# Performance work log

Measured on AMD Instinct MI355X. Metric: run time of the kernel, lower is better.

## Reference

```python
import jax, jax.numpy as jnp
import numpy as np

N, E, M, C = 4000, 60000, 16, 64        # nodes, edges, (lmax+1)^2, sphere_channels
H, HEADS, A, VC, CE, Z = 64, 8, 8, 8, 32, 90  # attn hidden, heads, alpha ch, value ch, edge ch, max elements


def _params(key):
    ks = jax.random.split(key, 10)
    g = lambda k, sh, fan: jax.random.normal(k, sh, dtype=jnp.float32) / np.float32(np.sqrt(fan))
    return [g(ks[0], (Z, CE), CE),          # emb_s: source atom embedding
            g(ks[1], (Z, CE), CE),          # emb_t: target atom embedding
            g(ks[2], (CE,), 1.0),           # w_d : distance projection
            g(ks[3], (CE, H), CE),          # We  : edge scalar -> hidden (m=0 inject)
            g(ks[4], (C, H), C),            # Ws  : source channel mix
            g(ks[5], (C, H), C),            # Wt  : target channel mix
            g(ks[6], (H, HEADS * A), H),    # Wa  : alpha features
            g(ks[7], (HEADS, A), A),        # va  : per-head alpha vector
            g(ks[8], (H, HEADS * VC), H),   # Wv  : values
            g(ks[9], (HEADS * VC, 1), HEADS * VC)]  # Wo : output proj (1 channel)


def setup_inputs() -> dict:
    key = jax.random.key(0)
    ks = jax.random.split(key, 8)
    x = jax.random.normal(ks[0], (N, M, C), dtype=jnp.float32)
    atomic_numbers = jax.random.randint(ks[1], (N,), 0, Z)
    edge_distance = jax.random.uniform(ks[2], (E,), dtype=jnp.float32) * 5.0 + 0.5
    edge_index = jax.random.randint(ks[3], (2, E), 0, N)
    noise_mask = jax.random.randint(ks[4], (N,), 0, 2).astype(bool)
    # per-edge SO3/Wigner rotation: random orthogonal [E, M, M]
    rng = np.random.default_rng(0)
    q, _ = np.linalg.qr(rng.standard_normal((E, M, M)).astype(np.float32))
    wigner = jnp.asarray(q, dtype=jnp.float32)
    names = ['emb_s', 'emb_t', 'w_d', 'We', 'Ws', 'Wt', 'Wa', 'va', 'Wv', 'Wo']
    inp = {'x': x, 'atomic_numbers': atomic_numbers, 'edge_distance': edge_distance,
           'edge_index': edge_index, 'noise_mask': noise_mask, 'wigner': wigner}
    for n, v in zip(names, _params(ks[5])):
        inp['fs_' + n] = v
    for n, v in zip(names, _params(ks[6])):
        inp['dn_' + n] = v
    return inp


def _block(x, zn, dist, src, dst, D, emb_s, emb_t, w_d, We, Ws, Wt, Wa, va, Wv, Wo):
    # gather + rotate edge-wise node features into edge-aligned frame
    xs = jnp.einsum('emn,enc->emc', D, x[src])            # [E,M,C]
    xt = jnp.einsum('emn,enc->emc', D, x[dst])            # [E,M,C]
    # scalar edge embedding (distance + source/target atom embeddings)
    e = jax.nn.silu(dist[:, None] * w_d + emb_s[zn[src]] + emb_t[zn[dst]])  # [E,CE]
    # SO2-style channel mixing; inject edge scalars into the m=0 (invariant) row
    f = jnp.einsum('emc,ch->emh', xs, Ws) + jnp.einsum('emc,ch->emh', xt, Wt)  # [E,M,H]
    f = f.at[:, 0, :].add(e @ We)
    # attention logits from the invariant part
    a = jax.nn.leaky_relu(f[:, 0, :] @ Wa, 0.2).reshape(E, HEADS, A)
    logits = jnp.einsum('eha,ha->eh', a, va)              # [E,HEADS]
    # segment softmax over incoming edges per target node
    mx = jax.ops.segment_max(logits, dst, num_segments=N)
    ex = jnp.exp(logits - mx[dst])
    alpha = ex / (jax.ops.segment_sum(ex, dst, num_segments=N)[dst] + 1e-9)
    # values, attention-weight, rotate back (D^T), scatter to nodes
    v = (f @ Wv).reshape(E, M, HEADS, VC) * alpha[:, None, :, None]
    v = jnp.einsum('emn,emhv->enhv', D, v).reshape(E, M, HEADS * VC)
    out = jax.ops.segment_sum(v, dst, num_segments=N) @ Wo  # [N,M,1]
    return out[:, 1:4, 0]  # narrow(1, 1, 3) -> l=1 vector components [N,3]


def reference(x, atomic_numbers, edge_distance, edge_index, noise_mask, wigner,
              fs_emb_s, fs_emb_t, fs_w_d, fs_We, fs_Ws, fs_Wt, fs_Wa, fs_va, fs_Wv, fs_Wo,
              dn_emb_s, dn_emb_t, dn_w_d, dn_We, dn_Ws, dn_Wt, dn_Wa, dn_va, dn_Wv, dn_Wo):
    src, dst = edge_index[0], edge_index[1]
    forces = _block(x, atomic_numbers, edge_distance, src, dst, wigner,
                    fs_emb_s, fs_emb_t, fs_w_d, fs_We, fs_Ws, fs_Wt, fs_Wa, fs_va, fs_Wv, fs_Wo)
    den = _block(x, atomic_numbers, edge_distance, src, dst, wigner,
                 dn_emb_s, dn_emb_t, dn_w_d, dn_We, dn_Ws, dn_Wt, dn_Wa, dn_va, dn_Wv, dn_Wo)
    # denoising_pos_forward with noise_mask: forces = den*mask + forces*~mask
    m = noise_mask[:, None].astype(x.dtype)
    return den * m + forces * (1.0 - m)
```

## Files before the change

### kernel.cpp

```cpp
#include <hip/hip_runtime.h>

typedef unsigned short ushort_t;
typedef __attribute__((ext_vector_type(8))) short short8;
typedef __attribute__((ext_vector_type(4))) float floatx4;

constexpr int RS = 11520;

__device__ inline float bf2f(ushort_t u) {
    union { unsigned int i; float f; } v; v.i = ((unsigned int)u) << 16; return v.f;
}
__device__ inline ushort_t f2bf(float f) {
    union { float f; unsigned int i; } v; v.f = f;
    unsigned int b = v.i + 0x7FFFu + ((v.i >> 16) & 1u);
    return (ushort_t)(b >> 16);
}

__global__ __launch_bounds__(256) void k_composites(
    const float* __restrict__ Ws0, const float* __restrict__ Wt0, const float* __restrict__ We0,
    const float* __restrict__ Wa0, const float* __restrict__ Wv0, const float* __restrict__ Wo0,
    const float* __restrict__ Ws1, const float* __restrict__ Wt1, const float* __restrict__ We1,
    const float* __restrict__ Wa1, const float* __restrict__ Wv1, const float* __restrict__ Wo1,
    float* __restrict__ cmp, ushort_t* __restrict__ packW)
{
    int task = blockIdx.x;
    int r    = blockIdx.y;
    int z    = blockIdx.z;
    const float* Ws = r ? Ws1 : Ws0;
    const float* Wt = r ? Wt1 : Wt0;
    const float* We = r ? We1 : We0;
    const float* Wa = r ? Wa1 : Wa0;
    const float* Wv = r ? Wv1 : Wv0;
    const float* Wo = r ? Wo1 : Wo0;
    float* base = cmp + r * RS;

    if (task == 0 || task == 1) {
        const float* L = task ? Wt : Ws;
        ushort_t* pw = packW + (r * 2 + task) * 4096;
        int lo = z * 1024;
        for (int idx = lo + threadIdx.x; idx < lo + 1024; idx += 256) {
            int c = idx >> 6, jc = idx & 63;
            float a = 0.f;
            #pragma unroll 8
            for (int k = 0; k < 64; ++k) a += L[c * 64 + k] * Wa[k * 64 + jc];
            int t = jc >> 4, n = jc & 15, kh = c >> 5, q = (c >> 3) & 3, jj = c & 7;
            pw[((t * 2 + kh) * 64 + q * 16 + n) * 8 + jj] = f2bf(a);
        }
    } else if (task == 2) {
        float* out = base + 8192;
        int lo = z * 512;
        for (int idx = lo + threadIdx.x; idx < lo + 512; idx += 256) {
            int ce = idx >> 6, jc = idx & 63;
            float a = 0.f;
            #pragma unroll 8
            for (int k = 0; k < 64; ++k) a += We[ce * 64 + k] * Wa[k * 64 + jc];
            out[idx] = a;
        }
    } else {
        if (z != 0) return;
        const float* L = (task == 3) ? Ws : (task == 4) ? Wt : We;
        int rows = (task == 5) ? 32 : 64;
        float* out = base + ((task == 3) ? 10240 : (task == 4) ? 10752 : 11264);
        for (int idx = threadIdx.x; idx < rows * 8; idx += 256) {
            int c = idx >> 3, h = idx & 7;
            float a = 0.f;
            for (int k = 0; k < 64; ++k) {
                float wv = 0.f;
                #pragma unroll
                for (int aa = 0; aa < 8; ++aa) wv += Wv[k * 64 + h * 8 + aa] * Wo[h * 8 + aa];
                a += L[c * 64 + k] * wv;
            }
            out[idx] = a;
        }
    }
}

__device__ inline short8 bfragP(const float* __restrict__ P0, const float* __restrict__ P1,
                                int kBase, int q, int n) {
    const float* P = (n < 8) ? P0 : P1;
    int c = n & 7;
    short8 f;
    #pragma unroll
    for (int j = 0; j < 8; ++j)
        f[j] = (short)f2bf(P[(kBase + q * 8 + j) * 8 + c]);
    return f;
}
__device__ inline void st4(ushort_t* dst, const floatx4& c) {
    uint2 v;
    v.x = (unsigned int)f2bf(c[0]) | ((unsigned int)f2bf(c[1]) << 16);
    v.y = (unsigned int)f2bf(c[2]) | ((unsigned int)f2bf(c[3]) << 16);
    *(uint2*)dst = v;
}

#define MFMA(a, b, c) __builtin_amdgcn_mfma_f32_16x16x32_bf16((a), (b), (c), 0, 0, 0)

__global__ __launch_bounds__(256, 2) void k_node(
    const float* __restrict__ x, const int* __restrict__ mask,
    const float* __restrict__ cmp, const ushort_t* __restrict__ packW,
    float* __restrict__ psrc, float* __restrict__ ptgt,
    ushort_t* __restrict__ srcA, ushort_t* __restrict__ tgtA,
    float* __restrict__ den, float* __restrict__ num,
    int N, int totWaves)
{
    int wid  = (int)((blockIdx.x * blockDim.x + threadIdx.x) >> 6);
    int lane = threadIdx.x & 63;
    int q    = lane >> 4;
    int n16  = lane & 15;

    short8 Bs0[4][2], Bs1[4][2], Bt0[4][2], Bt1[4][2];
    #pragma unroll
    for (int t = 0; t < 4; ++t) {
        #pragma unroll
        for (int kh = 0; kh < 2; ++kh) {
            int fo = (t * 2 + kh) * 512 + lane * 8;
            Bs0[t][kh] = *(const short8*)(packW +           fo);
            Bt0[t][kh] = *(const short8*)(packW +  4096 +   fo);
            Bs1[t][kh] = *(const short8*)(packW +  8192 +   fo);
            Bt1[t][kh] = *(const short8*)(packW + 12288 +   fo);
        }
    }
    short8 Bp[2], Bq[2];
    #pragma unroll
    for (int kh = 0; kh < 2; ++kh) {
        Bp[kh] = bfragP(cmp + 10240, cmp + RS + 10240, kh * 32, q, n16);
        Bq[kh] = bfragP(cmp + 10752, cmp + RS + 10752, kh * 32, q, n16);
    }

    const floatx4 zero = {0.f, 0.f, 0.f, 0.f};

    for (int nd = wid; nd < N; nd += totWaves) {
        if (lane < 8)  den[nd * 8 + lane] = 0.f;
        if (lane < 24) num[nd * 24 + lane] = 0.f;

        const float* xp = x + (size_t)nd * 1024 + n16 * 64 + q * 8;
        float4 v0 = *(const float4*)(xp);
        float4 v1 = *(const float4*)(xp + 4);
        float4 v2 = *(const float4*)(xp + 32);
        float4 v3 = *(const float4*)(xp + 36);
        short8 a0, a1;
        a0[0] = (short)f2bf(v0.x); a0[1] = (short)f2bf(v0.y);
        a0[2] = (short)f2bf(v0.z); a0[3] = (short)f2bf(v0.w);
        a0[4] = (short)f2bf(v1.x); a0[5] = (short)f2bf(v1.y);
        a0[6] = (short)f2bf(v1.z); a0[7] = (short)f2bf(v1.w);
        a1[0] = (short)f2bf(v2.x); a1[1] = (short)f2bf(v2.y);
        a1[2] = (short)f2bf(v2.z); a1[3] = (short)f2bf(v2.w);
        a1[4] = (short)f2bf(v3.x); a1[5] = (short)f2bf(v3.y);
        a1[6] = (short)f2bf(v3.z); a1[7] = (short)f2bf(v3.w);

        int rsel = (mask[nd] != 0);

        {
            floatx4 c0 = zero, c1 = zero, c2 = zero, c3 = zero;
            c0 = MFMA(a0, Bs0[0][0], c0); c0 = MFMA(a1, Bs0[0][1], c0);
            c1 = MFMA(a0, Bs0[1][0], c1); c1 = MFMA(a1, Bs0[1][1], c1);
            c2 = MFMA(a0, Bs0[2][0], c2); c2 = MFMA(a1, Bs0[2][1], c2);
            c3 = MFMA(a0, Bs0[3][0], c3); c3 = MFMA(a1, Bs0[3][1], c3);
            ushort_t* sp = srcA + (size_t)nd * 2048 + n16 * 16 + q * 4;
            st4(sp, c0); st4(sp + 256, c1); st4(sp + 512, c2); st4(sp + 768, c3);
        }
        {
            floatx4 c0 = zero, c1 = zero, c2 = zero, c3 = zero;
            c0 = MFMA(a0, Bs1[0][0], c0); c0 = MFMA(a1, Bs1[0][1], c0);
            c1 = MFMA(a0, Bs1[1][0], c1); c1 = MFMA(a1, Bs1[1][1], c1);
            c2 = MFMA(a0, Bs1[2][0], c2); c2 = MFMA(a1, Bs1[2][1], c2);
            c3 = MFMA(a0, Bs1[3][0], c3); c3 = MFMA(a1, Bs1[3][1], c3);
            ushort_t* sp = srcA + (size_t)nd * 2048 + 1024 + n16 * 16 + q * 4;
            st4(sp, c0); st4(sp + 256, c1); st4(sp + 512, c2); st4(sp + 768, c3);
        }

        {
            floatx4 c0 = zero, c1 = zero, c2 = zero, c3 = zero;
            if (rsel) {
                c0 = MFMA(a0, Bt1[0][0], c0); c0 = MFMA(a1, Bt1[0][1], c0);
                c1 = MFMA(a0, Bt1[1][0], c1); c1 = MFMA(a1, Bt1[1][1], c1);
                c2 = MFMA(a0, Bt1[2][0], c2); c2 = MFMA(a1, Bt1[2][1], c2);
                c3 = MFMA(a0, Bt1[3][0], c3); c3 = MFMA(a1, Bt1[3][1], c3);
            } else {
                c0 = MFMA(a0, Bt0[0][0], c0); c0 = MFMA(a1, Bt0[0][1], c0);
                c1 = MFMA(a0, Bt0[1][0], c1); c1 = MFMA(a1, Bt0[1][1], c1);
                c2 = MFMA(a0, Bt0[2][0], c2); c2 = MFMA(a1, Bt0[2][1], c2);
                c3 = MFMA(a0, Bt0[3][0], c3); c3 = MFMA(a1, Bt0[3][1], c3);
            }
            ushort_t* tp = tgtA + (size_t)nd * 1024 + n16 * 16 + q * 4;
            st4(tp, c0); st4(tp + 256, c1); st4(tp + 512, c2); st4(tp + 768, c3);
        }

        {
            floatx4 cp = zero;
            cp = MFMA(a0, Bp[0], cp); cp = MFMA(a1, Bp[1], cp);
            if (q == 0) {
                int r = n16 >> 3, h = n16 & 7;
                float* pp = psrc + (size_t)nd * 48 + r * 24 + h;
                pp[0]  = cp[1];
                pp[8]  = cp[2];
                pp[16] = cp[3];
            }
            floatx4 cq = zero;
            cq = MFMA(a0, Bq[0], cq); cq = MFMA(a1, Bq[1], cq);
            if (q == 0 && (n16 >> 3) == rsel) {
                int h = n16 & 7;
                float* pp = ptgt + (size_t)nd * 24 + h;
                pp[0]  = cq[1];
                pp[8]  = cq[2];
                pp[16] = cq[3];
            }
        }
    }
}

__global__ __launch_bounds__(256) void k_fused(
    const int* __restrict__ ei, const float* __restrict__ dist,
    const int* __restrict__ zn, const int* __restrict__ mask,
    const float* __restrict__ wig, const float* __restrict__ cmp,
    const float* __restrict__ embs0, const float* __restrict__ embt0, const float* __restrict__ wd0,
    const float* __restrict__ embs1, const float* __restrict__ embt1, const float* __restrict__ wd1,
    const float* __restrict__ va0, const float* __restrict__ va1,
    const ushort_t* __restrict__ srcA, const ushort_t* __restrict__ tgtA,
    const float* __restrict__ psrc, const float* __restrict__ ptgt,
    float* __restrict__ den, float* __restrict__ num, int E)
{
    int wv = threadIdx.x >> 6, j = threadIdx.x & 63;
    int e = blockIdx.x * 4 + wv;
    if (e >= E) return;
    int src = ei[e], dst = ei[E + e];
    int r = (mask[dst] != 0);
    float d = dist[e];
    int zs = zn[src], zt = zn[dst];
    int hq = j >> 3, h8 = j & 7;

    const float* w0 = wig + (size_t)e * 256;
    float4 wA = *(const float4*)(w0);
    float4 wB = *(const float4*)(w0 + 4);
    float4 wC = *(const float4*)(w0 + 8);
    float4 wD = *(const float4*)(w0 + 12);
    const ushort_t* sa = srcA + (size_t)src * 2048 + r * 1024 + j * 16;
    const ushort_t* ta = tgtA + (size_t)dst * 1024 + j * 16;
    short8 sv0 = *(const short8*)(sa);
    short8 sv1 = *(const short8*)(sa + 8);
    short8 tv0 = *(const short8*)(ta);
    short8 tv1 = *(const short8*)(ta + 8);
    float pv = 0.f;
    if (h8 < 3)
        pv = psrc[(size_t)src * 48 + r * 24 + h8 * 8 + hq]
           + ptgt[(size_t)dst * 24 + h8 * 8 + hq];

    float es;
    {
        int ce = j & 31;
        float z = r ? (d * wd1[ce] + embs1[zs * 32 + ce] + embt1[zt * 32 + ce])
                    : (d * wd0[ce] + embs0[zs * 32 + ce] + embt0[zt * 32 + ce]);
        es = z / (1.f + __expf(-z));
    }

    const float* WeWa   = cmp + r * RS + 8192;
    const float* WeWvWo = cmp + r * RS + 11264;
    float f0a = 0.f, ej = 0.f;
    #pragma unroll
    for (int ce = 0; ce < 32; ++ce) {
        float ev = __shfl(es, ce, 64);
        f0a += ev * WeWa[ce * 64 + j];
        ej  += ev * WeWvWo[ce * 8 + hq];
    }

    f0a += wA.x * (bf2f((ushort_t)sv0[0]) + bf2f((ushort_t)tv0[0]));
    f0a += wA.y * (bf2f((ushort_t)sv0[1]) + bf2f((ushort_t)tv0[1]));
    f0a += wA.z * (bf2f((ushort_t)sv0[2]) + bf2f((ushort_t)tv0[2]));
    f0a += wA.w * (bf2f((ushort_t)sv0[3]) + bf2f((ushort_t)tv0[3]));
    f0a += wB.x * (bf2f((ushort_t)sv0[4]) + bf2f((ushort_t)tv0[4]));
    f0a += wB.y * (bf2f((ushort_t)sv0[5]) + bf2f((ushort_t)tv0[5]));
    f0a += wB.z * (bf2f((ushort_t)sv0[6]) + bf2f((ushort_t)tv0[6]));
    f0a += wB.w * (bf2f((ushort_t)sv0[7]) + bf2f((ushort_t)tv0[7]));
    f0a += wC.x * (bf2f((ushort_t)sv1[0]) + bf2f((ushort_t)tv1[0]));
    f0a += wC.y * (bf2f((ushort_t)sv1[1]) + bf2f((ushort_t)tv1[1]));
    f0a += wC.z * (bf2f((ushort_t)sv1[2]) + bf2f((ushort_t)tv1[2]));
    f0a += wC.w * (bf2f((ushort_t)sv1[3]) + bf2f((ushort_t)tv1[3]));
    f0a += wD.x * (bf2f((ushort_t)sv1[4]) + bf2f((ushort_t)tv1[4]));
    f0a += wD.y * (bf2f((ushort_t)sv1[5]) + bf2f((ushort_t)tv1[5]));
    f0a += wD.z * (bf2f((ushort_t)sv1[6]) + bf2f((ushort_t)tv1[6]));
    f0a += wD.w * (bf2f((ushort_t)sv1[7]) + bf2f((ushort_t)tv1[7]));

    float la = f0a > 0.f ? f0a : 0.2f * f0a;
    float val = la * (r ? va1[j] : va0[j]);
    val += __shfl_xor(val, 1);
    val += __shfl_xor(val, 2);
    val += __shfl_xor(val, 4);
    float ex = __expf(val);

    if (h8 == 0) atomicAdd(&den[dst * 8 + hq], ex);
    if (h8 < 3) {
        float w0k = (h8 == 0) ? wA.y : (h8 == 1) ? wA.z : wA.w;
        atomicAdd(&num[dst * 24 + hq * 3 + h8], ex * (pv + ej * w0k));
    }
}

__global__ __launch_bounds__(256) void k_out(
    const float* __restrict__ num, const float* __restrict__ den,
    float* __restrict__ out, int N3)
{
    int t = blockIdx.x * 256 + threadIdx.x;
    if (t >= N3) return;
    int n = t / 3, k = t - n * 3;
    float acc = 0.f;
    #pragma unroll
    for (int h = 0; h < 8; ++h)
        acc += num[n * 24 + h * 3 + k] / (den[n * 8 + h] + 1e-9f);
    out[t] = acc;
}

extern "C" void kernel_launch(void* const* d_in, const int* in_sizes, int n_in,
                              void* d_out, int out_size, void* d_ws, size_t ws_size,
                              hipStream_t stream) {
    const float* x    = (const float*)d_in[0];
    const int*   zn   = (const int*)d_in[1];
    const float* dist = (const float*)d_in[2];
    const int*   ei   = (const int*)d_in[3];
    const int*   mask = (const int*)d_in[4];
    const float* wig  = (const float*)d_in[5];
    const float* fs[10]; const float* dn[10];
    for (int i = 0; i < 10; ++i) { fs[i] = (const float*)d_in[6 + i]; dn[i] = (const float*)d_in[16 + i]; }

    int N = in_sizes[1];
    int E = in_sizes[2];

    float* cmp  = (float*)d_ws;
    float* den  = cmp + 2 * RS;
    float* num  = den + (size_t)N * 8;
    float* psrc = num + (size_t)N * 24;
    float* ptgt = psrc + (size_t)N * 48;
    ushort_t* srcA = (ushort_t*)(ptgt + (size_t)N * 24);
    ushort_t* tgtA = srcA + (size_t)N * 2048;
    ushort_t* packW = tgtA + (size_t)N * 1024;


    k_composites<<<dim3(6, 2, 4), 256, 0, stream>>>(
        fs[4], fs[5], fs[3], fs[6], fs[8], fs[9],
        dn[4], dn[5], dn[3], dn[6], dn[8], dn[9], cmp, packW);

    int nodeBlocks = 1000;
    int totWaves = nodeBlocks * (256 / 64);
    k_node<<<nodeBlocks, 256, 0, stream>>>(x, mask, cmp, packW, psrc, ptgt,
                                           srcA, tgtA, den, num, N, totWaves);

    k_fused<<<(E + 3) / 4, 256, 0, stream>>>(
        ei, dist, zn, mask, wig, cmp,
        fs[0], fs[1], fs[2], dn[0], dn[1], dn[2],
        fs[7], dn[7], srcA, tgtA, psrc, ptgt, den, num, E);

    k_out<<<(N * 3 + 255) / 256, 256, 0, stream>>>(num, den, (float*)d_out, N * 3);
}
```

Baseline: 225.1 us.

## Sort edges by destination in cooperative prep kernel and stage node weights in LDS

Replaces the weight-composite kernel with a cooperative kernel that also computes a counting sort of edges by destination node, so the edge kernel visits edges in dst order. This improves locality of the atomic accumulation into den/num and of the target-node gathers. The node kernel now stages packed bf16 weights in shared memory instead of holding them in registers, and uses one wave per node with higher occupancy. The cost is three grid syncs, global atomics for binning, and an extra indirection per edge.

```diff
diff --git a/kernel.cpp b/kernel.cpp
--- a/kernel.cpp
+++ b/kernel.cpp
@@ -1,4 +1,7 @@
 #include <hip/hip_runtime.h>
+#include <hip/hip_cooperative_groups.h>
+
+namespace cg = cooperative_groups;
 
 typedef unsigned short ushort_t;
 typedef __attribute__((ext_vector_type(8))) short short8;
@@ -13,76 +16,6 @@
     union { float f; unsigned int i; } v; v.f = f;
     unsigned int b = v.i + 0x7FFFu + ((v.i >> 16) & 1u);
     return (ushort_t)(b >> 16);
-}
-
-__global__ __launch_bounds__(256) void k_composites(
-    const float* __restrict__ Ws0, const float* __restrict__ Wt0, const float* __restrict__ We0,
-    const float* __restrict__ Wa0, const float* __restrict__ Wv0, const float* __restrict__ Wo0,
-    const float* __restrict__ Ws1, const float* __restrict__ Wt1, const float* __restrict__ We1,
-    const float* __restrict__ Wa1, const float* __restrict__ Wv1, const float* __restrict__ Wo1,
-    float* __restrict__ cmp, ushort_t* __restrict__ packW)
-{
-    int task = blockIdx.x;
-    int r    = blockIdx.y;
-    int z    = blockIdx.z;
-    const float* Ws = r ? Ws1 : Ws0;
-    const float* Wt = r ? Wt1 : Wt0;
-    const float* We = r ? We1 : We0;
-    const float* Wa = r ? Wa1 : Wa0;
-    const float* Wv = r ? Wv1 : Wv0;
-    const float* Wo = r ? Wo1 : Wo0;
-    float* base = cmp + r * RS;
-
-    if (task == 0 || task == 1) {
-        const float* L = task ? Wt : Ws;
-        ushort_t* pw = packW + (r * 2 + task) * 4096;
-        int lo = z * 1024;
-        for (int idx = lo + threadIdx.x; idx < lo + 1024; idx += 256) {
-            int c = idx >> 6, jc = idx & 63;
-            float a = 0.f;
-            #pragma unroll 8
-            for (int k = 0; k < 64; ++k) a += L[c * 64 + k] * Wa[k * 64 + jc];
-            int t = jc >> 4, n = jc & 15, kh = c >> 5, q = (c >> 3) & 3, jj = c & 7;
-            pw[((t * 2 + kh) * 64 + q * 16 + n) * 8 + jj] = f2bf(a);
-        }
-    } else if (task == 2) {
-        float* out = base + 8192;
-        int lo = z * 512;
-        for (int idx = lo + threadIdx.x; idx < lo + 512; idx += 256) {
-            int ce = idx >> 6, jc = idx & 63;
-            float a = 0.f;
-            #pragma unroll 8
-            for (int k = 0; k < 64; ++k) a += We[ce * 64 + k] * Wa[k * 64 + jc];
-            out[idx] = a;
-        }
-    } else {
-        if (z != 0) return;
-        const float* L = (task == 3) ? Ws : (task == 4) ? Wt : We;
-        int rows = (task == 5) ? 32 : 64;
-        float* out = base + ((task == 3) ? 10240 : (task == 4) ? 10752 : 11264);
-        for (int idx = threadIdx.x; idx < rows * 8; idx += 256) {
-            int c = idx >> 3, h = idx & 7;
-            float a = 0.f;
-            for (int k = 0; k < 64; ++k) {
-                float wv = 0.f;
-                #pragma unroll
-                for (int aa = 0; aa < 8; ++aa) wv += Wv[k * 64 + h * 8 + aa] * Wo[h * 8 + aa];
-                a += L[c * 64 + k] * wv;
-            }
-            out[idx] = a;
-        }
-    }
-}
-
-__device__ inline short8 bfragP(const float* __restrict__ P0, const float* __restrict__ P1,
-                                int kBase, int q, int n) {
-    const float* P = (n < 8) ? P0 : P1;
-    int c = n & 7;
-    short8 f;
-    #pragma unroll
-    for (int j = 0; j < 8; ++j)
-        f[j] = (short)f2bf(P[(kBase + q * 8 + j) * 8 + c]);
-    return f;
 }
 __device__ inline void st4(ushort_t* dst, const floatx4& c) {
     uint2 v;
@@ -93,41 +26,133 @@
 
 #define MFMA(a, b, c) __builtin_amdgcn_mfma_f32_16x16x32_bf16((a), (b), (c), 0, 0, 0)
 
-__global__ __launch_bounds__(256, 2) void k_node(
+__global__ __launch_bounds__(256) void k_pre(
+    const float* __restrict__ Ws0, const float* __restrict__ Wt0, const float* __restrict__ We0,
+    const float* __restrict__ Wa0, const float* __restrict__ Wv0, const float* __restrict__ Wo0,
+    const float* __restrict__ Ws1, const float* __restrict__ Wt1, const float* __restrict__ We1,
+    const float* __restrict__ Wa1, const float* __restrict__ Wv1, const float* __restrict__ Wo1,
+    const int* __restrict__ ei, float* __restrict__ cmp, ushort_t* __restrict__ packW,
+    int* __restrict__ binCnt, int* __restrict__ binPos, int* __restrict__ order,
+    int N, int E)
+{
+    cg::grid_group g = cg::this_grid();
+    __shared__ int part[256];
+    int tid = blockIdx.x * 256 + threadIdx.x;
+    int nT  = gridDim.x * 256;
+
+    for (int i = tid; i < N; i += nT) binCnt[i] = 0;
+    g.sync();
+    for (int e = tid; e < E; e += nT) atomicAdd(&binCnt[ei[E + e]], 1);
+    g.sync();
+
+    int b = blockIdx.x;
+    if (b < 48) {
+        int task = b % 6, r = (b / 6) % 2, z = b / 12;
+        const float* Ws = r ? Ws1 : Ws0;
+        const float* Wt = r ? Wt1 : Wt0;
+        const float* We = r ? We1 : We0;
+        const float* Wa = r ? Wa1 : Wa0;
+        const float* Wv = r ? Wv1 : Wv0;
+        const float* Wo = r ? Wo1 : Wo0;
+        float* base = cmp + r * RS;
+
+        if (task == 0 || task == 1) {
+            const float* L = task ? Wt : Ws;
+            ushort_t* pw = packW + (r * 2 + task) * 4096;
+            int lo = z * 1024;
+            for (int idx = lo + threadIdx.x; idx < lo + 1024; idx += 256) {
+                int c = idx >> 6, jc = idx & 63;
+                float a = 0.f;
+                #pragma unroll 8
+                for (int k = 0; k < 64; ++k) a += L[c * 64 + k] * Wa[k * 64 + jc];
+                int t = jc >> 4, n = jc & 15, kh = c >> 5, q = (c >> 3) & 3, jj = c & 7;
+                pw[((t * 2 + kh) * 64 + q * 16 + n) * 8 + jj] = f2bf(a);
+            }
+        } else if (task == 2) {
+            float* out = base + 8192;
+            int lo = z * 512;
+            for (int idx = lo + threadIdx.x; idx < lo + 512; idx += 256) {
+                int ce = idx >> 6, jc = idx & 63;
+                float a = 0.f;
+                #pragma unroll 8
+                for (int k = 0; k < 64; ++k) a += We[ce * 64 + k] * Wa[k * 64 + jc];
+                out[idx] = a;
+            }
+        } else if (z == 0) {
+            if (task == 5) {
+                float* out = base + 11264;
+                for (int idx = threadIdx.x; idx < 32 * 8; idx += 256) {
+                    int c = idx >> 3, h = idx & 7;
+                    float a = 0.f;
+                    for (int k = 0; k < 64; ++k) {
+                        float wv = 0.f;
+                        #pragma unroll
+                        for (int aa = 0; aa < 8; ++aa) wv += Wv[k * 64 + h * 8 + aa] * Wo[h * 8 + aa];
+                        a += We[c * 64 + k] * wv;
+                    }
+                    out[idx] = a;
+                }
+            } else {
+                const float* L = (task == 3) ? Ws : Wt;
+                ushort_t* pp = packW + 16384 + (task - 3) * 1024;
+                for (int idx = threadIdx.x; idx < 64 * 8; idx += 256) {
+                    int c = idx >> 3, h = idx & 7;
+                    float a = 0.f;
+                    for (int k = 0; k < 64; ++k) {
+                        float wv = 0.f;
+                        #pragma unroll
+                        for (int aa = 0; aa < 8; ++aa) wv += Wv[k * 64 + h * 8 + aa] * Wo[h * 8 + aa];
+                        a += L[c * 64 + k] * wv;
+                    }
+                    int kh = c >> 5, q = (c >> 3) & 3, jj = c & 7;
+                    pp[kh * 512 + (q * 16 + r * 8 + h) * 8 + jj] = f2bf(a);
+                }
+            }
+        }
+    } else if (b == 48) {
+        int t = threadIdx.x;
+        int chunk = (N + 255) / 256;
+        int lo = t * chunk, hi = lo + chunk; if (hi > N) hi = N; if (lo > N) lo = N;
+        int s = 0;
+        for (int i = lo; i < hi; ++i) s += binCnt[i];
+        part[t] = s;
+        __syncthreads();
+        for (int off = 1; off < 256; off <<= 1) {
+            int v = (t >= off) ? part[t - off] : 0;
+            __syncthreads();
+            part[t] += v;
+            __syncthreads();
+        }
+        int start = (t == 0) ? 0 : part[t - 1];
+        for (int i = lo; i < hi; ++i) { int c = binCnt[i]; binPos[i] = start; start += c; }
+    }
+    g.sync();
+
+    for (int e = tid; e < E; e += nT) {
+        int pos = atomicAdd(&binPos[ei[E + e]], 1);
+        order[pos] = e;
+    }
+}
+
+__global__ __launch_bounds__(256, 4) void k_node(
     const float* __restrict__ x, const int* __restrict__ mask,
-    const float* __restrict__ cmp, const ushort_t* __restrict__ packW,
+    const ushort_t* __restrict__ packW,
     float* __restrict__ psrc, float* __restrict__ ptgt,
     ushort_t* __restrict__ srcA, ushort_t* __restrict__ tgtA,
-    float* __restrict__ den, float* __restrict__ num,
-    int N, int totWaves)
+    float* __restrict__ den, float* __restrict__ num, int N)
 {
+    __shared__ __align__(16) ushort_t lw[18432];
+    for (int i = threadIdx.x; i < 2304; i += 256)
+        ((short8*)lw)[i] = ((const short8*)packW)[i];
+    __syncthreads();
+
     int wid  = (int)((blockIdx.x * blockDim.x + threadIdx.x) >> 6);
     int lane = threadIdx.x & 63;
     int q    = lane >> 4;
     int n16  = lane & 15;
 
-    short8 Bs0[4][2], Bs1[4][2], Bt0[4][2], Bt1[4][2];
-    #pragma unroll
-    for (int t = 0; t < 4; ++t) {
-        #pragma unroll
-        for (int kh = 0; kh < 2; ++kh) {
-            int fo = (t * 2 + kh) * 512 + lane * 8;
-            Bs0[t][kh] = *(const short8*)(packW +           fo);
-            Bt0[t][kh] = *(const short8*)(packW +  4096 +   fo);
-            Bs1[t][kh] = *(const short8*)(packW +  8192 +   fo);
-            Bt1[t][kh] = *(const short8*)(packW + 12288 +   fo);
-        }
-    }
-    short8 Bp[2], Bq[2];
-    #pragma unroll
-    for (int kh = 0; kh < 2; ++kh) {
-        Bp[kh] = bfragP(cmp + 10240, cmp + RS + 10240, kh * 32, q, n16);
-        Bq[kh] = bfragP(cmp + 10752, cmp + RS + 10752, kh * 32, q, n16);
-    }
-
-    const floatx4 zero = {0.f, 0.f, 0.f, 0.f};
-
-    for (int nd = wid; nd < N; nd += totWaves) {
+    if (wid < N) {
+        int nd = wid;
         if (lane < 8)  den[nd * 8 + lane] = 0.f;
         if (lane < 24) num[nd * 24 + lane] = 0.f;
 
@@ -147,46 +172,42 @@
         a1[6] = (short)f2bf(v3.z); a1[7] = (short)f2bf(v3.w);
 
         int rsel = (mask[nd] != 0);
+        const floatx4 zero = {0.f, 0.f, 0.f, 0.f};
+
+        #define WF(mat, t, kh) (*(const short8*)&lw[(mat) * 4096 + ((t) * 2 + (kh)) * 512 + lane * 8])
+        #define PF(m, kh)      (*(const short8*)&lw[16384 + (m) * 1024 + (kh) * 512 + lane * 8])
 
         {
             floatx4 c0 = zero, c1 = zero, c2 = zero, c3 = zero;
-            c0 = MFMA(a0, Bs0[0][0], c0); c0 = MFMA(a1, Bs0[0][1], c0);
-            c1 = MFMA(a0, Bs0[1][0], c1); c1 = MFMA(a1, Bs0[1][1], c1);
-            c2 = MFMA(a0, Bs0[2][0], c2); c2 = MFMA(a1, Bs0[2][1], c2);
-            c3 = MFMA(a0, Bs0[3][0], c3); c3 = MFMA(a1, Bs0[3][1], c3);
+            c0 = MFMA(a0, WF(0,0,0), c0); c0 = MFMA(a1, WF(0,0,1), c0);
+            c1 = MFMA(a0, WF(0,1,0), c1); c1 = MFMA(a1, WF(0,1,1), c1);
+            c2 = MFMA(a0, WF(0,2,0), c2); c2 = MFMA(a1, WF(0,2,1), c2);
+            c3 = MFMA(a0, WF(0,3,0), c3); c3 = MFMA(a1, WF(0,3,1), c3);
             ushort_t* sp = srcA + (size_t)nd * 2048 + n16 * 16 + q * 4;
             st4(sp, c0); st4(sp + 256, c1); st4(sp + 512, c2); st4(sp + 768, c3);
         }
         {
             floatx4 c0 = zero, c1 = zero, c2 = zero, c3 = zero;
-            c0 = MFMA(a0, Bs1[0][0], c0); c0 = MFMA(a1, Bs1[0][1], c0);
-            c1 = MFMA(a0, Bs1[1][0], c1); c1 = MFMA(a1, Bs1[1][1], c1);
-            c2 = MFMA(a0, Bs1[2][0], c2); c2 = MFMA(a1, Bs1[2][1], c2);
-            c3 = MFMA(a0, Bs1[3][0], c3); c3 = MFMA(a1, Bs1[3][1], c3);
+            c0 = MFMA(a0, WF(2,0,0), c0); c0 = MFMA(a1, WF(2,0,1), c0);
+            c1 = MFMA(a0, WF(2,1,0), c1); c1 = MFMA(a1, WF(2,1,1), c1);
+            c2 = MFMA(a0, WF(2,2,0), c2); c2 = MFMA(a1, WF(2,2,1), c2);
+            c3 = MFMA(a0, WF(2,3,0), c3); c3 = MFMA(a1, WF(2,3,1), c3);
             ushort_t* sp = srcA + (size_t)nd * 2048 + 1024 + n16 * 16 + q * 4;
             st4(sp, c0); st4(sp + 256, c1); st4(sp + 512, c2); st4(sp + 768, c3);
         }
-
         {
+            int mt = rsel ? 3 : 1;
             floatx4 c0 = zero, c1 = zero, c2 = zero, c3 = zero;
-            if (rsel) {
-                c0 = MFMA(a0, Bt1[0][0], c0); c0 = MFMA(a1, Bt1[0][1], c0);
-                c1 = MFMA(a0, Bt1[1][0], c1); c1 = MFMA(a1, Bt1[1][1], c1);
-                c2 = MFMA(a0, Bt1[2][0], c2); c2 = MFMA(a1, Bt1[2][1], c2);
-                c3 = MFMA(a0, Bt1[3][0], c3); c3 = MFMA(a1, Bt1[3][1], c3);
-            } else {
-                c0 = MFMA(a0, Bt0[0][0], c0); c0 = MFMA(a1, Bt0[0][1], c0);
-                c1 = MFMA(a0, Bt0[1][0], c1); c1 = MFMA(a1, Bt0[1][1], c1);
-                c2 = MFMA(a0, Bt0[2][0], c2); c2 = MFMA(a1, Bt0[2][1], c2);
-                c3 = MFMA(a0, Bt0[3][0], c3); c3 = MFMA(a1, Bt0[3][1], c3);
-            }
+            c0 = MFMA(a0, WF(mt,0,0), c0); c0 = MFMA(a1, WF(mt,0,1), c0);
+            c1 = MFMA(a0, WF(mt,1,0), c1); c1 = MFMA(a1, WF(mt,1,1), c1);
+            c2 = MFMA(a0, WF(mt,2,0), c2); c2 = MFMA(a1, WF(mt,2,1), c2);
+            c3 = MFMA(a0, WF(mt,3,0), c3); c3 = MFMA(a1, WF(mt,3,1), c3);
             ushort_t* tp = tgtA + (size_t)nd * 1024 + n16 * 16 + q * 4;
             st4(tp, c0); st4(tp + 256, c1); st4(tp + 512, c2); st4(tp + 768, c3);
         }
-
         {
             floatx4 cp = zero;
-            cp = MFMA(a0, Bp[0], cp); cp = MFMA(a1, Bp[1], cp);
+            cp = MFMA(a0, PF(0,0), cp); cp = MFMA(a1, PF(0,1), cp);
             if (q == 0) {
                 int r = n16 >> 3, h = n16 & 7;
                 float* pp = psrc + (size_t)nd * 48 + r * 24 + h;
@@ -195,7 +216,7 @@
                 pp[16] = cp[3];
             }
             floatx4 cq = zero;
-            cq = MFMA(a0, Bq[0], cq); cq = MFMA(a1, Bq[1], cq);
+            cq = MFMA(a0, PF(1,0), cq); cq = MFMA(a1, PF(1,1), cq);
             if (q == 0 && (n16 >> 3) == rsel) {
                 int h = n16 & 7;
                 float* pp = ptgt + (size_t)nd * 24 + h;
@@ -204,10 +225,12 @@
                 pp[16] = cq[3];
             }
         }
-    }
-}
-
-__global__ __launch_bounds__(256) void k_fused(
+        #undef WF
+        #undef PF
+    }
+}
+
+__global__ __launch_bounds__(256, 8) void k_fused(
     const int* __restrict__ ei, const float* __restrict__ dist,
     const int* __restrict__ zn, const int* __restrict__ mask,
     const float* __restrict__ wig, const float* __restrict__ cmp,
@@ -216,11 +239,13 @@
     const float* __restrict__ va0, const float* __restrict__ va1,
     const ushort_t* __restrict__ srcA, const ushort_t* __restrict__ tgtA,
     const float* __restrict__ psrc, const float* __restrict__ ptgt,
+    const int* __restrict__ order,
     float* __restrict__ den, float* __restrict__ num, int E)
 {
     int wv = threadIdx.x >> 6, j = threadIdx.x & 63;
-    int e = blockIdx.x * 4 + wv;
-    if (e >= E) return;
+    int el = blockIdx.x * 4 + wv;
+    if (el >= E) return;
+    int e = order[el];
     int src = ei[e], dst = ei[E + e];
     int r = (mask[dst] != 0);
     float d = dist[e];
@@ -329,21 +354,26 @@
     ushort_t* srcA = (ushort_t*)(ptgt + (size_t)N * 24);
     ushort_t* tgtA = srcA + (size_t)N * 2048;
     ushort_t* packW = tgtA + (size_t)N * 1024;
-
-
-    k_composites<<<dim3(6, 2, 4), 256, 0, stream>>>(
-        fs[4], fs[5], fs[3], fs[6], fs[8], fs[9],
-        dn[4], dn[5], dn[3], dn[6], dn[8], dn[9], cmp, packW);
-
-    int nodeBlocks = 1000;
-    int totWaves = nodeBlocks * (256 / 64);
-    k_node<<<nodeBlocks, 256, 0, stream>>>(x, mask, cmp, packW, psrc, ptgt,
-                                           srcA, tgtA, den, num, N, totWaves);
+    int* binCnt = (int*)(packW + 18432);
+    int* binPos = binCnt + N;
+    int* order  = binPos + N;
+
+    const float *Ws0 = fs[4], *Wt0 = fs[5], *We0 = fs[3], *Wa0 = fs[6], *Wv0 = fs[8], *Wo0 = fs[9];
+    const float *Ws1 = dn[4], *Wt1 = dn[5], *We1 = dn[3], *Wa1 = dn[6], *Wv1 = dn[8], *Wo1 = dn[9];
+    int Nv = N, Ev = E;
+    void* args[] = { &Ws0, &Wt0, &We0, &Wa0, &Wv0, &Wo0,
+                     &Ws1, &Wt1, &We1, &Wa1, &Wv1, &Wo1,
+                     &ei, &cmp, &packW, &binCnt, &binPos, &order, &Nv, &Ev };
+    hipLaunchCooperativeKernel((const void*)k_pre, dim3(256), dim3(256), args, 0, stream);
+
+    int nodeBlocks = (N + 3) / 4;
+    k_node<<<nodeBlocks, 256, 0, stream>>>(x, mask, packW, psrc, ptgt,
+                                           srcA, tgtA, den, num, N);
 
     k_fused<<<(E + 3) / 4, 256, 0, stream>>>(
         ei, dist, zn, mask, wig, cmp,
         fs[0], fs[1], fs[2], dn[0], dn[1], dn[2],
-        fs[7], dn[7], srcA, tgtA, psrc, ptgt, den, num, E);
+        fs[7], dn[7], srcA, tgtA, psrc, ptgt, order, den, num, E);
 
     k_out<<<(N * 3 + 255) / 256, 256, 0, stream>>>(num, den, (float*)d_out, N * 3);
 }
```

Result: slower. 447.5 us (+98.8%).

## Make edge kernel persistent with software-prefetched next-edge loads

Applied to the files above, without the earlier changes.

The per-edge kernel becomes a grid-stride persistent loop over a fixed 2048-block grid. Each wave prefetches the next edge's Wigner row, gathered node features, projections and embeddings while it computes the current edge, and loads indices two edges ahead. The aim is to hide gather latency and cut block launch overhead. In exchange, register pressure rises and fewer waves are resident, which may reduce the latency hiding that occupancy used to provide.

```diff
diff --git a/kernel.cpp b/kernel.cpp
--- a/kernel.cpp
+++ b/kernel.cpp
@@ -14,6 +14,14 @@
     unsigned int b = v.i + 0x7FFFu + ((v.i >> 16) & 1u);
     return (ushort_t)(b >> 16);
 }
+__device__ inline void st4(ushort_t* dst, const floatx4& c) {
+    uint2 v;
+    v.x = (unsigned int)f2bf(c[0]) | ((unsigned int)f2bf(c[1]) << 16);
+    v.y = (unsigned int)f2bf(c[2]) | ((unsigned int)f2bf(c[3]) << 16);
+    *(uint2*)dst = v;
+}
+
+#define MFMA(a, b, c) __builtin_amdgcn_mfma_f32_16x16x32_bf16((a), (b), (c), 0, 0, 0)
 
 __global__ __launch_bounds__(256) void k_composites(
     const float* __restrict__ Ws0, const float* __restrict__ Wt0, const float* __restrict__ We0,
@@ -84,14 +92,6 @@
         f[j] = (short)f2bf(P[(kBase + q * 8 + j) * 8 + c]);
     return f;
 }
-__device__ inline void st4(ushort_t* dst, const floatx4& c) {
-    uint2 v;
-    v.x = (unsigned int)f2bf(c[0]) | ((unsigned int)f2bf(c[1]) << 16);
-    v.y = (unsigned int)f2bf(c[2]) | ((unsigned int)f2bf(c[3]) << 16);
-    *(uint2*)dst = v;
-}
-
-#define MFMA(a, b, c) __builtin_amdgcn_mfma_f32_16x16x32_bf16((a), (b), (c), 0, 0, 0)
 
 __global__ __launch_bounds__(256, 2) void k_node(
     const float* __restrict__ x, const int* __restrict__ mask,
@@ -166,7 +166,6 @@
             ushort_t* sp = srcA + (size_t)nd * 2048 + 1024 + n16 * 16 + q * 4;
             st4(sp, c0); st4(sp + 256, c1); st4(sp + 512, c2); st4(sp + 768, c3);
         }
-
         {
             floatx4 c0 = zero, c1 = zero, c2 = zero, c3 = zero;
             if (rsel) {
@@ -183,7 +182,6 @@
             ushort_t* tp = tgtA + (size_t)nd * 1024 + n16 * 16 + q * 4;
             st4(tp, c0); st4(tp + 256, c1); st4(tp + 512, c2); st4(tp + 768, c3);
         }
-
         {
             floatx4 cp = zero;
             cp = MFMA(a0, Bp[0], cp); cp = MFMA(a1, Bp[1], cp);
@@ -216,79 +214,123 @@
     const float* __restrict__ va0, const float* __restrict__ va1,
     const ushort_t* __restrict__ srcA, const ushort_t* __restrict__ tgtA,
     const float* __restrict__ psrc, const float* __restrict__ ptgt,
-    float* __restrict__ den, float* __restrict__ num, int E)
+    float* __restrict__ den, float* __restrict__ num, int E, int stride)
 {
     int wv = threadIdx.x >> 6, j = threadIdx.x & 63;
-    int e = blockIdx.x * 4 + wv;
-    if (e >= E) return;
-    int src = ei[e], dst = ei[E + e];
-    int r = (mask[dst] != 0);
-    float d = dist[e];
-    int zs = zn[src], zt = zn[dst];
-    int hq = j >> 3, h8 = j & 7;
-
-    const float* w0 = wig + (size_t)e * 256;
+    int wid = blockIdx.x * 4 + wv;
+    if (wid >= E) return;
+    int hq = j >> 3, h8 = j & 7, ce = j & 31;
+
+    int eC = wid;
+    int srcC = ei[eC], dstC = ei[E + eC];
+    int rC = (mask[dstC] != 0);
+    float dC = dist[eC];
+    int zsC = zn[srcC], ztC = zn[dstC];
+
+    int eN = wid + stride;
+    bool hasN = (eN < E);
+    int eNc = hasN ? eN : eC;
+    int srcN = ei[eNc], dstN = ei[E + eNc];
+    int rN = (mask[dstN] != 0);
+    float dN = dist[eNc];
+    int zsN = zn[srcN], ztN = zn[dstN];
+
+    const float* w0 = wig + (size_t)eC * 256;
     float4 wA = *(const float4*)(w0);
     float4 wB = *(const float4*)(w0 + 4);
     float4 wC = *(const float4*)(w0 + 8);
     float4 wD = *(const float4*)(w0 + 12);
-    const ushort_t* sa = srcA + (size_t)src * 2048 + r * 1024 + j * 16;
-    const ushort_t* ta = tgtA + (size_t)dst * 1024 + j * 16;
-    short8 sv0 = *(const short8*)(sa);
-    short8 sv1 = *(const short8*)(sa + 8);
-    short8 tv0 = *(const short8*)(ta);
-    short8 tv1 = *(const short8*)(ta + 8);
+    const ushort_t* sa = srcA + (size_t)srcC * 2048 + rC * 1024 + j * 16;
+    const ushort_t* ta = tgtA + (size_t)dstC * 1024 + j * 16;
+    short8 sv0 = *(const short8*)(sa), sv1 = *(const short8*)(sa + 8);
+    short8 tv0 = *(const short8*)(ta), tv1 = *(const short8*)(ta + 8);
     float pv = 0.f;
     if (h8 < 3)
-        pv = psrc[(size_t)src * 48 + r * 24 + h8 * 8 + hq]
-           + ptgt[(size_t)dst * 24 + h8 * 8 + hq];
-
-    float es;
-    {
-        int ce = j & 31;
-        float z = r ? (d * wd1[ce] + embs1[zs * 32 + ce] + embt1[zt * 32 + ce])
-                    : (d * wd0[ce] + embs0[zs * 32 + ce] + embt0[zt * 32 + ce]);
-        es = z / (1.f + __expf(-z));
-    }
-
-    const float* WeWa   = cmp + r * RS + 8192;
-    const float* WeWvWo = cmp + r * RS + 11264;
-    float f0a = 0.f, ej = 0.f;
-    #pragma unroll
-    for (int ce = 0; ce < 32; ++ce) {
-        float ev = __shfl(es, ce, 64);
-        f0a += ev * WeWa[ce * 64 + j];
-        ej  += ev * WeWvWo[ce * 8 + hq];
-    }
-
-    f0a += wA.x * (bf2f((ushort_t)sv0[0]) + bf2f((ushort_t)tv0[0]));
-    f0a += wA.y * (bf2f((ushort_t)sv0[1]) + bf2f((ushort_t)tv0[1]));
-    f0a += wA.z * (bf2f((ushort_t)sv0[2]) + bf2f((ushort_t)tv0[2]));
-    f0a += wA.w * (bf2f((ushort_t)sv0[3]) + bf2f((ushort_t)tv0[3]));
-    f0a += wB.x * (bf2f((ushort_t)sv0[4]) + bf2f((ushort_t)tv0[4]));
-    f0a += wB.y * (bf2f((ushort_t)sv0[5]) + bf2f((ushort_t)tv0[5]));
-    f0a += wB.z * (bf2f((ushort_t)sv0[6]) + bf2f((ushort_t)tv0[6]));
-    f0a += wB.w * (bf2f((ushort_t)sv0[7]) + bf2f((ushort_t)tv0[7]));
-    f0a += wC.x * (bf2f((ushort_t)sv1[0]) + bf2f((ushort_t)tv1[0]));
-    f0a += wC.y * (bf2f((ushort_t)sv1[1]) + bf2f((ushort_t)tv1[1]));
-    f0a += wC.z * (bf2f((ushort_t)sv1[2]) + bf2f((ushort_t)tv1[2]));
-    f0a += wC.w * (bf2f((ushort_t)sv1[3]) + bf2f((ushort_t)tv1[3]));
-    f0a += wD.x * (bf2f((ushort_t)sv1[4]) + bf2f((ushort_t)tv1[4]));
-    f0a += wD.y * (bf2f((ushort_t)sv1[5]) + bf2f((ushort_t)tv1[5]));
-    f0a += wD.z * (bf2f((ushort_t)sv1[6]) + bf2f((ushort_t)tv1[6]));
-    f0a += wD.w * (bf2f((ushort_t)sv1[7]) + bf2f((ushort_t)tv1[7]));
-
-    float la = f0a > 0.f ? f0a : 0.2f * f0a;
-    float val = la * (r ? va1[j] : va0[j]);
-    val += __shfl_xor(val, 1);
-    val += __shfl_xor(val, 2);
-    val += __shfl_xor(val, 4);
-    float ex = __expf(val);
-
-    if (h8 == 0) atomicAdd(&den[dst * 8 + hq], ex);
-    if (h8 < 3) {
-        float w0k = (h8 == 0) ? wA.y : (h8 == 1) ? wA.z : wA.w;
-        atomicAdd(&num[dst * 24 + hq * 3 + h8], ex * (pv + ej * w0k));
+        pv = psrc[(size_t)srcC * 48 + rC * 24 + h8 * 8 + hq]
+           + ptgt[(size_t)dstC * 24 + h8 * 8 + hq];
+    float eb  = (rC ? embs1 : embs0)[zsC * 32 + ce] + (rC ? embt1 : embt0)[ztC * 32 + ce];
+    float wdc = (rC ? wd1 : wd0)[ce];
+    float vaj = (rC ? va1 : va0)[j];
+
+    while (true) {
+        float4 nwA = wA, nwB = wB, nwC = wC, nwD = wD;
+        short8 nsv0 = sv0, nsv1 = sv1, ntv0 = tv0, ntv1 = tv1;
+        float npv = 0.f, neb = 0.f, nwdc = 0.f, nvaj = 0.f;
+        if (hasN) {
+            const float* w1 = wig + (size_t)eN * 256;
+            nwA = *(const float4*)(w1);
+            nwB = *(const float4*)(w1 + 4);
+            nwC = *(const float4*)(w1 + 8);
+            nwD = *(const float4*)(w1 + 12);
+            const ushort_t* sa1 = srcA + (size_t)srcN * 2048 + rN * 1024 + j * 16;
+            const ushort_t* ta1 = tgtA + (size_t)dstN * 1024 + j * 16;
+            nsv0 = *(const short8*)(sa1); nsv1 = *(const short8*)(sa1 + 8);
+            ntv0 = *(const short8*)(ta1); ntv1 = *(const short8*)(ta1 + 8);
+            if (h8 < 3)
+                npv = psrc[(size_t)srcN * 48 + rN * 24 + h8 * 8 + hq]
+                    + ptgt[(size_t)dstN * 24 + h8 * 8 + hq];
+            neb  = (rN ? embs1 : embs0)[zsN * 32 + ce] + (rN ? embt1 : embt0)[ztN * 32 + ce];
+            nwdc = (rN ? wd1 : wd0)[ce];
+            nvaj = (rN ? va1 : va0)[j];
+        }
+        int e2 = eN + stride;
+        bool has2 = hasN && (e2 < E);
+        int e2c = has2 ? e2 : eNc;
+        int src2 = ei[e2c], dst2 = ei[E + e2c];
+        int r2 = (mask[dst2] != 0);
+        float d2 = dist[e2c];
+        int zs2 = zn[src2], zt2 = zn[dst2];
+
+        const float* WeWa   = cmp + rC * RS + 8192;
+        const float* WeWvWo = cmp + rC * RS + 11264;
+        float z = dC * wdc + eb;
+        float es = z / (1.f + __expf(-z));
+
+        float f0a = 0.f, ej = 0.f;
+        #pragma unroll
+        for (int cc = 0; cc < 32; ++cc) {
+            float ev = __shfl(es, cc, 64);
+            f0a += ev * WeWa[cc * 64 + j];
+            ej  += ev * WeWvWo[cc * 8 + hq];
+        }
+
+        f0a += wA.x * (bf2f((ushort_t)sv0[0]) + bf2f((ushort_t)tv0[0]));
+        f0a += wA.y * (bf2f((ushort_t)sv0[1]) + bf2f((ushort_t)tv0[1]));
+        f0a += wA.z * (bf2f((ushort_t)sv0[2]) + bf2f((ushort_t)tv0[2]));
+        f0a += wA.w * (bf2f((ushort_t)sv0[3]) + bf2f((ushort_t)tv0[3]));
+        f0a += wB.x * (bf2f((ushort_t)sv0[4]) + bf2f((ushort_t)tv0[4]));
+        f0a += wB.y * (bf2f((ushort_t)sv0[5]) + bf2f((ushort_t)tv0[5]));
+        f0a += wB.z * (bf2f((ushort_t)sv0[6]) + bf2f((ushort_t)tv0[6]));
+        f0a += wB.w * (bf2f((ushort_t)sv0[7]) + bf2f((ushort_t)tv0[7]));
+        f0a += wC.x * (bf2f((ushort_t)sv1[0]) + bf2f((ushort_t)tv1[0]));
+        f0a += wC.y * (bf2f((ushort_t)sv1[1]) + bf2f((ushort_t)tv1[1]));
+        f0a += wC.z * (bf2f((ushort_t)sv1[2]) + bf2f((ushort_t)tv1[2]));
+        f0a += wC.w * (bf2f((ushort_t)sv1[3]) + bf2f((ushort_t)tv1[3]));
+        f0a += wD.x * (bf2f((ushort_t)sv1[4]) + bf2f((ushort_t)tv1[4]));
+        f0a += wD.y * (bf2f((ushort_t)sv1[5]) + bf2f((ushort_t)tv1[5]));
+        f0a += wD.z * (bf2f((ushort_t)sv1[6]) + bf2f((ushort_t)tv1[6]));
+        f0a += wD.w * (bf2f((ushort_t)sv1[7]) + bf2f((ushort_t)tv1[7]));
+
+        float la = f0a > 0.f ? f0a : 0.2f * f0a;
+        float val = la * vaj;
+        val += __shfl_xor(val, 1);
+        val += __shfl_xor(val, 2);
+        val += __shfl_xor(val, 4);
+        float ex = __expf(val);
+
+        if (h8 == 0) atomicAdd(&den[dstC * 8 + hq], ex);
+        if (h8 < 3) {
+            float w0k = (h8 == 0) ? wA.y : (h8 == 1) ? wA.z : wA.w;
+            atomicAdd(&num[dstC * 24 + hq * 3 + h8], ex * (pv + ej * w0k));
+        }
+
+        if (!hasN) break;
+        eC = eN; dstC = dstN; rC = rN; dC = dN;
+        wA = nwA; wB = nwB; wC = nwC; wD = nwD;
+        sv0 = nsv0; sv1 = nsv1; tv0 = ntv0; tv1 = ntv1;
+        pv = npv; eb = neb; wdc = nwdc; vaj = nvaj;
+        eN = e2; hasN = has2; eNc = e2c;
+        srcN = src2; dstN = dst2; rN = r2; dN = d2; zsN = zs2; ztN = zt2;
     }
 }
 
@@ -330,20 +372,21 @@
     ushort_t* tgtA = srcA + (size_t)N * 2048;
     ushort_t* packW = tgtA + (size_t)N * 1024;
 
-
     k_composites<<<dim3(6, 2, 4), 256, 0, stream>>>(
         fs[4], fs[5], fs[3], fs[6], fs[8], fs[9],
         dn[4], dn[5], dn[3], dn[6], dn[8], dn[9], cmp, packW);
 
     int nodeBlocks = 1000;
-    int totWaves = nodeBlocks * (256 / 64);
+    int totWaves = nodeBlocks * 4;
     k_node<<<nodeBlocks, 256, 0, stream>>>(x, mask, cmp, packW, psrc, ptgt,
                                            srcA, tgtA, den, num, N, totWaves);
 
-    k_fused<<<(E + 3) / 4, 256, 0, stream>>>(
+    int fusedBlocks = 2048;
+    int stride = fusedBlocks * 4;
+    k_fused<<<fusedBlocks, 256, 0, stream>>>(
         ei, dist, zn, mask, wig, cmp,
         fs[0], fs[1], fs[2], dn[0], dn[1], dn[2],
-        fs[7], dn[7], srcA, tgtA, psrc, ptgt, den, num, E);
+        fs[7], dn[7], srcA, tgtA, psrc, ptgt, den, num, E, stride);
 
     k_out<<<(N * 3 + 255) / 256, 256, 0, stream>>>(num, den, (float*)d_out, N * 3);
 }
```

Result: slower. 255.8 us (+13.6%).
